# Kernel tuning notes

Measured on AMD Instinct MI355X. Metric: run time of the kernel, lower is better.

Reference implementation:

```python
import jax, jax.numpy as jnp
import numpy as np

BATCH = 512
HIDDEN_DIM = 4096
NUM_CODES = 32
CODE_DIM = 64
CODEBOOK_SIZE = 1024


def _lsa_single(cost):
    """Rectangular Hungarian (Jonker-Volgenant shortest augmenting path).
    cost: [n, m] with n <= m. Returns, for each row, the assigned column,
    minimizing total cost (matches scipy.optimize.linear_sum_assignment)."""
    n, m = cost.shape
    u = np.zeros(n + 1)
    v = np.zeros(m + 1)
    p = np.zeros(m + 1, dtype=np.int64)  # p[j]: row matched to col j (1-based); 0 = free
    for i in range(1, n + 1):
        p[0] = i
        j0 = 0
        minv = np.full(m + 1, np.inf)
        way = np.zeros(m + 1, dtype=np.int64)
        used = np.zeros(m + 1, dtype=bool)
        while True:
            used[j0] = True
            i0 = p[j0]
            free = ~used
            free[0] = False
            jfree = np.nonzero(free)[0]
            cur = cost[i0 - 1, jfree - 1] - u[i0] - v[jfree]
            upd = cur < minv[jfree]
            minv[jfree[upd]] = cur[upd]
            way[jfree[upd]] = j0
            k = jfree[np.argmin(minv[jfree])]
            delta = minv[k]
            u[p[used]] += delta
            v[used] -= delta
            minv[free] -= delta
            j0 = k
            if p[j0] == 0:
                break
        while j0 != 0:  # augment along the path
            j1 = way[j0]
            p[j0] = p[j1]
            j0 = j1
    ans = np.empty(n, dtype=np.int64)
    for j in range(1, m + 1):
        if p[j] > 0:
            ans[p[j] - 1] = j - 1
    return ans


def _lsa_batch(costs):
    costs = np.asarray(costs, dtype=np.float64)
    return np.stack([_lsa_single(c) for c in costs]).astype(np.int32)


def setup_inputs() -> dict:
    key = jax.random.key(0)
    ks = jax.random.split(key, 4)
    return {
        "x": jax.random.normal(ks[0], (BATCH, HIDDEN_DIM), jnp.float32),
        "codebook": jax.random.normal(ks[1], (CODEBOOK_SIZE, CODE_DIM), jnp.float32),
        "enc_w": jax.random.normal(ks[2], (NUM_CODES * CODE_DIM, HIDDEN_DIM), jnp.float32) * 0.02,
        "enc_b": jnp.zeros((NUM_CODES * CODE_DIM,), jnp.float32),
        "dec_w": jax.random.normal(ks[3], (HIDDEN_DIM, NUM_CODES * CODE_DIM), jnp.float32) * 0.02,
        "dec_b": jnp.zeros((HIDDEN_DIM,), jnp.float32),
    }


def reference(x, codebook, enc_w, enc_b, dec_w, dec_b):
    bs = x.shape[0]
    # encoder (torch Linear: y = x @ W.T + b)
    e = (x @ enc_w.T + enc_b).reshape(bs, NUM_CODES, CODE_DIM)
    ef = e.reshape(-1, CODE_DIM)  # [bs*num_codes, code_dim]
    # pairwise Euclidean distances to codebook entries [bs*num_codes, codebook_size]
    d2 = (jnp.sum(ef * ef, axis=1, keepdims=True)
          + jnp.sum(codebook * codebook, axis=1)
          - 2.0 * (ef @ codebook.T))
    dist = jnp.sqrt(jnp.maximum(d2, 0.0)).reshape(bs, NUM_CODES, CODEBOOK_SIZE)
    # per-sample Hungarian assignment (original uses scipy on CPU; sqrt is
    # monotone so the optimal assignment is identical)
    indices = jax.pure_callback(
        _lsa_batch,
        jax.ShapeDtypeStruct((bs, NUM_CODES), jnp.int32),
        jax.lax.stop_gradient(dist),
    )
    flat_idx = indices.reshape(-1)  # matches torch's concatenated flat indices
    q = codebook[flat_idx].reshape(bs, NUM_CODES, CODE_DIM)
    # straight-through estimator
    q_st = e + jax.lax.stop_gradient(q - e)
    r = q_st.reshape(bs, NUM_CODES * CODE_DIM) @ dec_w.T + dec_b
    return (r, q, e, flat_idx)
```

## Files before the change

### kernel.cpp

```cpp
#include <hip/hip_runtime.h>
#include <hip/hip_bf16.h>
#include <stdint.h>

#define BATCH 512
#define HID   4096
#define NC    32
#define CD    64
#define CB    1024
#define NCD   2048

typedef unsigned short u16;
typedef unsigned int   u32;
typedef __attribute__((ext_vector_type(8))) short short8;
typedef __attribute__((ext_vector_type(4))) float f32x4;

#define WAVE_SYNC()  asm volatile("s_waitcnt lgkmcnt(0)" ::: "memory")
#define SCHED_FENCE() __builtin_amdgcn_sched_barrier(0)

__device__ inline u16 bf16_rne(float f) {
  u32 u = __builtin_bit_cast(u32, f);
  u32 r = u + 0x7FFFu + ((u >> 16) & 1u);
  return (u16)(r >> 16);
}
__device__ inline float bf16_f32(u16 h) {
  u32 u = ((u32)h) << 16;
  return __builtin_bit_cast(float, u);
}
__device__ inline void split3(float a, u16& h1, u16& h2, u16& h3) {
  h1 = bf16_rne(a);
  float r1 = a - bf16_f32(h1);
  h2 = bf16_rne(r1);
  float r2 = r1 - bf16_f32(h2);
  h3 = bf16_rne(r2);
}
__device__ inline f32x4 mfma16(short8 a, short8 b, f32x4 c) {
  return __builtin_amdgcn_mfma_f32_16x16x32_bf16(a, b, c, 0, 0, 0);
}
__device__ inline void gload_lds16(const u16* g, u16* l) {
  __builtin_amdgcn_global_load_lds(
      (const __attribute__((address_space(1))) u32*)(const void*)g,
      (__attribute__((address_space(3))) u32*)(void*)l, 16, 0, 0);
}

union H8 { u16 h[8]; short8 v; };

template<int K>
__global__ __launch_bounds__(256) void conv_split3(
    const float* __restrict__ src, u16* __restrict__ d1,
    u16* __restrict__ d2, u16* __restrict__ d3) {
  __shared__ float st[4][16][36];
  const int t = threadIdx.x;
  const int wv = t >> 6, l = t & 63;
  const int g = blockIdx.x * 4 + wv;
  const int rowbase = (g / (K / 32)) * 16;
  const int kbase   = (g % (K / 32)) * 32;
  {
    const float* s = src + (size_t)(rowbase + (l >> 2)) * K + kbase + (l & 3) * 8;
    *(f32x4*)&st[wv][l >> 2][(l & 3) * 8]     = *(const f32x4*)s;
    *(f32x4*)&st[wv][l >> 2][(l & 3) * 8 + 4] = *(const f32x4*)(s + 4);
  }
  __syncthreads();
  float vv[8];
  *(f32x4*)&vv[0] = *(const f32x4*)&st[wv][l & 15][(l >> 4) * 8];
  *(f32x4*)&vv[4] = *(const f32x4*)&st[wv][l & 15][(l >> 4) * 8 + 4];
  H8 o1, o2, o3;
#pragma unroll
  for (int i = 0; i < 8; ++i) split3(vv[i], o1.h[i], o2.h[i], o3.h[i]);
  size_t off = (size_t)g * 512 + l * 8;
  *(short8*)(d1 + off) = o1.v;
  *(short8*)(d2 + off) = o2.v;
  *(short8*)(d3 + off) = o3.v;
}

template<int K>
__global__ __launch_bounds__(256) void conv_split1(
    const float* __restrict__ src, u16* __restrict__ d1) {
  __shared__ float st[4][16][36];
  const int t = threadIdx.x;
  const int wv = t >> 6, l = t & 63;
  const int g = blockIdx.x * 4 + wv;
  const int rowbase = (g / (K / 32)) * 16;
  const int kbase   = (g % (K / 32)) * 32;
  {
    const float* s = src + (size_t)(rowbase + (l >> 2)) * K + kbase + (l & 3) * 8;
    *(f32x4*)&st[wv][l >> 2][(l & 3) * 8]     = *(const f32x4*)s;
    *(f32x4*)&st[wv][l >> 2][(l & 3) * 8 + 4] = *(const f32x4*)(s + 4);
  }
  __syncthreads();
  float vv[8];
  *(f32x4*)&vv[0] = *(const f32x4*)&st[wv][l & 15][(l >> 4) * 8];
  *(f32x4*)&vv[4] = *(const f32x4*)&st[wv][l & 15][(l >> 4) * 8 + 4];
  H8 o1;
#pragma unroll
  for (int i = 0; i < 8; ++i) o1.h[i] = bf16_rne(vv[i]);
  *(short8*)(d1 + (size_t)g * 512 + l * 8) = o1.v;
}

__global__ __launch_bounds__(256, 2) void k1_gemm(
    const u16* __restrict__ A1, const u16* __restrict__ A2,
    const u16* __restrict__ A3,
    const u16* __restrict__ B1, const u16* __restrict__ B2,
    const u16* __restrict__ B3, float* __restrict__ part) {
  __shared__ u16 lds_all[72 * 512];
  const int t = threadIdx.x;
  const int wid = t >> 6, lane = t & 63;
  const int wrow = wid >> 1, wcol = wid & 1;
  const int d = blockIdx.x + (blockIdx.y << 2) + (blockIdx.z << 7);
  const int xcd = d & 7, sl = d >> 3;
  const int panel = (xcd << 4) + (sl >> 2);
  const int bm = (sl & 3) * 128;
  const int bn_t = panel & 31;
  const int kz = panel >> 5;
  const int ks0 = kz * 32;

  const u16* gp[9];
#pragma unroll
  for (int i = 0; i < 9; ++i) {
    const int b = wid + 4 * i;
    const u16* base;
    size_t frag;
    if (b < 24) {
      const int s = b >> 3, rf = b & 7;
      base = (s == 0) ? A1 : (s == 1) ? A2 : A3;
      frag = (size_t)((bm >> 4) + rf);
    } else {
      const int bb = b - 24;
      const int s = bb >> 2, cf = bb & 3;
      base = (s == 0) ? B1 : (s == 1) ? B2 : B3;
      frag = (size_t)(bn_t * 4 + cf);
    }
    gp[i] = base + (frag * 128 + ks0) * 512 + lane * 8;
  }

  f32x4 acc[4][2];
#pragma unroll
  for (int r = 0; r < 4; ++r)
#pragma unroll
    for (int c = 0; c < 2; ++c) acc[r][c] = (f32x4)0.f;

  for (int ks = 0; ks < 16; ++ks) {
#pragma unroll
    for (int i = 0; i < 9; ++i) {
      const int b = wid + 4 * i;
      gload_lds16(gp[i],       &lds_all[b * 512]);
      gload_lds16(gp[i] + 512, &lds_all[(36 + b) * 512]);
      gp[i] += 1024;
    }
    __syncthreads();
#pragma unroll
    for (int ss = 0; ss < 2; ++ss) {
      const int o = ss * 36;
      short8 b0[2], b1[2], b2[2];
#pragma unroll
      for (int c = 0; c < 2; ++c) {
        const int cf = wcol * 2 + c;
        b0[c] = *(const short8*)&lds_all[(o + 24 + 0 * 4 + cf) * 512 + lane * 8];
        b1[c] = *(const short8*)&lds_all[(o + 24 + 1 * 4 + cf) * 512 + lane * 8];
        b2[c] = *(const short8*)&lds_all[(o + 24 + 2 * 4 + cf) * 512 + lane * 8];
      }
#pragma unroll
      for (int r = 0; r < 4; ++r) {
        const int rf = wrow * 4 + r;
        short8 a0 = *(const short8*)&lds_all[(o + 0 * 8 + rf) * 512 + lane * 8];
        short8 a1 = *(const short8*)&lds_all[(o + 1 * 8 + rf) * 512 + lane * 8];
        short8 a2 = *(const short8*)&lds_all[(o + 2 * 8 + rf) * 512 + lane * 8];
#pragma unroll
        for (int c = 0; c < 2; ++c) {
          f32x4 dd = acc[r][c];
          dd = mfma16(a0, b0[c], dd);
          dd = mfma16(a0, b1[c], dd);
          dd = mfma16(a1, b0[c], dd);
          dd = mfma16(a1, b1[c], dd);
          dd = mfma16(a0, b2[c], dd);
          dd = mfma16(a2, b0[c], dd);
          acc[r][c] = dd;
        }
      }
    }
    __syncthreads();
  }
  float* P = part + (size_t)kz * BATCH * NCD;
#pragma unroll
  for (int r = 0; r < 4; ++r)
#pragma unroll
    for (int c = 0; c < 2; ++c) {
      int row = bm + wrow * 64 + r * 16 + (lane >> 4) * 4;
      int col = bn_t * 64 + wcol * 32 + c * 16 + (lane & 15);
#pragma unroll
      for (int i = 0; i < 4; ++i)
        P[(size_t)(row + i) * NCD + col] = acc[r][c][i];
    }
}

__global__ __launch_bounds__(256) void k_reduce_bias(
    const float* __restrict__ part, const float* __restrict__ bias,
    float* __restrict__ e) {
  size_t o = ((size_t)blockIdx.x * 256 + threadIdx.x) * 4;
  int n = (int)(o & (NCD - 1));
  f32x4 s = *(const f32x4*)(part + o);
  s += *(const f32x4*)(part + (size_t)1 * BATCH * NCD + o);
  s += *(const f32x4*)(part + (size_t)2 * BATCH * NCD + o);
  s += *(const f32x4*)(part + (size_t)3 * BATCH * NCD + o);
  s += *(const f32x4*)(bias + n);
  *(f32x4*)(e + o) = s;
}

__global__ __launch_bounds__(512) void k3_gemm(
    const u16* __restrict__ Ab, const u16* __restrict__ Bb,
    const float* __restrict__ bias, float* __restrict__ C) {
  __shared__ u16 As[4][64][8];
  __shared__ u16 Bs[8][64][8];
  const int t = threadIdx.x;
  const int wid = t >> 6, lane = t & 63;
  const int wrow = wid >> 2, wcol = wid & 3;
  const int d = blockIdx.x + (blockIdx.y << 3);
  const int xcd = d & 7, sl = d >> 3;
  const int bn = ((xcd << 2) + (sl >> 3)) * 128;
  const int bm = (sl & 7) * 64;
  f32x4 acc[2][2];
#pragma unroll
  for (int r = 0; r < 2; ++r)
#pragma unroll
    for (int c = 0; c < 2; ++c) acc[r][c] = (f32x4)0.f;

  for (int ks = 0; ks < 64; ++ks) {
    {
      size_t gb = (((size_t)(bn >> 4) + wid) * 64 + ks) * 512 + lane * 8;
      gload_lds16(Bb + gb, &Bs[wid][0][0]);
      if (wid < 4) {
        size_t ga = (((size_t)(bm >> 4) + wid) * 64 + ks) * 512 + lane * 8;
        gload_lds16(Ab + ga, &As[wid][0][0]);
      }
    }
    __syncthreads();
    short8 a[2], b[2];
#pragma unroll
    for (int r = 0; r < 2; ++r) a[r] = *(const short8*)&As[wrow * 2 + r][lane][0];
#pragma unroll
    for (int c = 0; c < 2; ++c) b[c] = *(const short8*)&Bs[wcol * 2 + c][lane][0];
#pragma unroll
    for (int r = 0; r < 2; ++r)
#pragma unroll
      for (int c = 0; c < 2; ++c) acc[r][c] = mfma16(a[r], b[c], acc[r][c]);
    __syncthreads();
  }
#pragma unroll
  for (int r = 0; r < 2; ++r)
#pragma unroll
    for (int c = 0; c < 2; ++c) {
      int row = bm + wrow * 32 + r * 16 + (lane >> 4) * 4;
      int col = bn + wcol * 32 + c * 16 + (lane & 15);
      float bb = bias[col];
#pragma unroll
      for (int i = 0; i < 4; ++i)
        C[(size_t)(row + i) * HID + col] = acc[r][c][i] + bb;
    }
}

__global__ __launch_bounds__(512) void k_cost(
    const float* __restrict__ e_glob,
    const float* __restrict__ codebook,
    float* __restrict__ cost) {
  __shared__ u16 Ea[2][3][8][64][8];
  __shared__ u16 Cbs[2][3][8][64][8];
  __shared__ float enorm[128], cnorm[128];
  const int t = threadIdx.x;
  const int wid = t >> 6, lane = t & 63;
  const int wrow = wid >> 2, wcol = wid & 3;
  const int r0 = blockIdx.x * 128;
  const int c0 = blockIdx.y * 128;

  {
    const int fr = lane & 15, kc = lane >> 4;
    const float* ea = e_glob   + (size_t)(r0 + wid * 16 + fr) * CD + kc * 8;
    const float* cb = codebook + (size_t)(c0 + wid * 16 + fr) * CD + kc * 8;
#pragma unroll
    for (int ks = 0; ks < 2; ++ks) {
      float va[8], vb[8];
      *(f32x4*)&va[0] = *(const f32x4*)(ea + ks * 32);
      *(f32x4*)&va[4] = *(const f32x4*)(ea + ks * 32 + 4);
      *(f32x4*)&vb[0] = *(const f32x4*)(cb + ks * 32);
      *(f32x4*)&vb[4] = *(const f32x4*)(cb + ks * 32 + 4);
      H8 a1, a2, a3, b1, b2, b3;
#pragma unroll
      for (int i = 0; i < 8; ++i) {
        split3(va[i], a1.h[i], a2.h[i], a3.h[i]);
        split3(vb[i], b1.h[i], b2.h[i], b3.h[i]);
      }
      *(short8*)&Ea[ks][0][wid][lane][0] = a1.v;
      *(short8*)&Ea[ks][1][wid][lane][0] = a2.v;
      *(short8*)&Ea[ks][2][wid][lane][0] = a3.v;
      *(short8*)&Cbs[ks][0][wid][lane][0] = b1.v;
      *(short8*)&Cbs[ks][1][wid][lane][0] = b2.v;
      *(short8*)&Cbs[ks][2][wid][lane][0] = b3.v;
    }
  }
  if (t < 256) {
    const int which = t >> 7, idx = t & 127;
    const float* p = which ? codebook + (size_t)(c0 + idx) * CD
                           : e_glob   + (size_t)(r0 + idx) * CD;
    float s = 0.f;
#pragma unroll
    for (int k = 0; k < 16; ++k) {
      f32x4 v = *(const f32x4*)(p + k * 4);
      s += v.x * v.x + v.y * v.y + v.z * v.z + v.w * v.w;
    }
    if (which) cnorm[idx] = s; else enorm[idx] = s;
  }
  __syncthreads();

  f32x4 acc[4][2];
#pragma unroll
  for (int r = 0; r < 4; ++r)
#pragma unroll
    for (int c = 0; c < 2; ++c) acc[r][c] = (f32x4)0.f;
#pragma unroll
  for (int ks = 0; ks < 2; ++ks) {
    short8 a0[4], a1[4], a2[4], b0[2], b1[2], b2[2];
#pragma unroll
    for (int r = 0; r < 4; ++r) {
      a0[r] = *(const short8*)&Ea[ks][0][wrow * 4 + r][lane][0];
      a1[r] = *(const short8*)&Ea[ks][1][wrow * 4 + r][lane][0];
      a2[r] = *(const short8*)&Ea[ks][2][wrow * 4 + r][lane][0];
    }
#pragma unroll
    for (int c = 0; c < 2; ++c) {
      b0[c] = *(const short8*)&Cbs[ks][0][wcol * 2 + c][lane][0];
      b1[c] = *(const short8*)&Cbs[ks][1][wcol * 2 + c][lane][0];
      b2[c] = *(const short8*)&Cbs[ks][2][wcol * 2 + c][lane][0];
    }
#pragma unroll
    for (int r = 0; r < 4; ++r)
#pragma unroll
      for (int c = 0; c < 2; ++c) {
        f32x4 dd = acc[r][c];
        dd = mfma16(a0[r], b0[c], dd);
        dd = mfma16(a0[r], b1[c], dd);
        dd = mfma16(a1[r], b0[c], dd);
        dd = mfma16(a1[r], b1[c], dd);
        dd = mfma16(a0[r], b2[c], dd);
        dd = mfma16(a2[r], b0[c], dd);
        acc[r][c] = dd;
      }
  }
#pragma unroll
  for (int r = 0; r < 4; ++r)
#pragma unroll
    for (int c = 0; c < 2; ++c) {
      const int rl = wrow * 64 + r * 16 + (lane >> 4) * 4;
      const int cl = wcol * 32 + c * 16 + (lane & 15);
      const float cn = cnorm[cl];
#pragma unroll
      for (int i = 0; i < 4; ++i) {
        float d2 = enorm[rl + i] + cn - 2.f * acc[r][c][i];
        cost[(size_t)(r0 + rl + i) * CB + c0 + cl] = sqrtf(fmaxf(d2, 0.f));
      }
    }
}

__global__ __launch_bounds__(64, 1) void k_assign(
    const float* __restrict__ cost_g, const float* __restrict__ codebook,
    float* __restrict__ q_out, float* __restrict__ idx_out) {
  __shared__ int idxl[32];
  const int lane = threadIdx.x;
  const int s = blockIdx.x;
  const float* __restrict__ cost = cost_g + (size_t)s * NC * CB;

  double v_[16], minv_[16];
  u32 wp_[16];
  double u_val = 0.0;
#pragma unroll
  for (int r = 0; r < 16; ++r) { v_[r] = 0.0; wp_[r] = 0; }

  float pf[16];
#pragma unroll
  for (int r = 0; r < 16; ++r) pf[r] = cost[r * 64 + lane];

  for (int i = 1; i <= NC; ++i) {
#pragma unroll
    for (int r = 0; r < 16; ++r) minv_[r] = 1e300;
    u32 col_used = 0;
    unsigned long long rowmask = 0ull;
    int j0 = 0;
    int i0 = i;
    float cc[16];
#pragma unroll
    for (int r = 0; r < 16; ++r) cc[r] = pf[r];
    int first = 1;
    for (int guard = 0; guard < 1056; ++guard) {
      rowmask |= (1ull << i0);
      const double ui0 = __shfl(u_val, i0);
      if (first && i < NC) {
#pragma unroll
        for (int r = 0; r < 16; ++r)
          pf[r] = cost[(size_t)i * CB + r * 64 + lane];
      }
      first = 0;
      double bv = 1e301; int bj = 1 << 20;
#pragma unroll
      for (int r = 0; r < 16; ++r) {
        const int j = 1 + lane + r * 64;
        if (!((col_used >> r) & 1u)) {
          double cur = (double)cc[r] - ui0 - v_[r];
          if (cur < minv_[r]) { minv_[r] = cur; wp_[r] = (wp_[r] & 0xFFFF0000u) | (u32)j0; }
          if (minv_[r] < bv) { bv = minv_[r]; bj = j; }
        }
      }
#pragma unroll
      for (int off = 1; off < 64; off <<= 1) {
        double ov = __shfl_xor(bv, off);
        int oj = __shfl_xor(bj, off);
        if (ov < bv || (ov == bv && oj < bj)) { bv = ov; bj = oj; }
      }
      const double delta = bv;
      const int k = bj;
      const int rk = (k - 1) >> 6, kl = (k - 1) & 63;
      u32 sel = 0;
#pragma unroll
      for (int r = 0; r < 16; ++r) if (r == rk) sel = wp_[r];
      const int pmk = ((u32)__shfl((int)sel, kl)) >> 16;
      float ccn[16];
      if (pmk > 0) {
        const float* crow = cost + (size_t)(pmk - 1) * CB;
#pragma unroll
        for (int r = 0; r < 16; ++r) ccn[r] = crow[r * 64 + lane];
      }
      if ((rowmask >> lane) & 1ull) u_val += delta;
#pragma unroll
      for (int r = 0; r < 16; ++r) {
        const int j = 1 + lane + r * 64;
        if ((col_used >> r) & 1u) v_[r] -= delta;
        else {
          minv_[r] -= delta;
          if (j == k) col_used |= (1u << r);
        }
      }
      j0 = k;
      if (pmk == 0) break;
      i0 = pmk;
#pragma unroll
      for (int r = 0; r < 16; ++r) cc[r] = ccn[r];
    }
    int jj = j0;
    while (jj != 0) {
      const int rj = (jj - 1) >> 6, lj = (jj - 1) & 63;
      u32 wsel = 0;
#pragma unroll
      for (int r = 0; r < 16; ++r) if (r == rj) wsel = wp_[r];
      const int j1 = ((u32)__shfl((int)wsel, lj)) & 0xFFFFu;
      int newpm;
      if (j1 == 0) newpm = i;
      else {
        const int r1 = (j1 - 1) >> 6, l1 = (j1 - 1) & 63;
        u32 psel = 0;
#pragma unroll
        for (int r = 0; r < 16; ++r) if (r == r1) psel = wp_[r];
        newpm = ((u32)__shfl((int)psel, l1)) >> 16;
      }
#pragma unroll
      for (int r = 0; r < 16; ++r)
        if (lane == lj && r == rj) wp_[r] = (wp_[r] & 0xFFFFu) | ((u32)newpm << 16);
      jj = j1;
    }
  }

#pragma unroll
  for (int r = 0; r < 16; ++r) {
    const u32 pm = wp_[r] >> 16;
    if (pm > 0) idxl[pm - 1] = lane + r * 64;
  }
  WAVE_SYNC(); SCHED_FENCE();
  if (lane < NC) idx_out[(size_t)s * NC + lane] = (float)idxl[lane];
#pragma unroll
  for (int p = 0; p < 8; ++p) {
    int vi = p * 64 + lane;
    int r = vi >> 4, c4 = vi & 15;
    int ci = idxl[r];
    float4 qv = *(const float4*)&codebook[(size_t)ci * 64 + c4 * 4];
    *(float4*)&q_out[(size_t)s * NCD + r * 64 + c4 * 4] = qv;
  }
}

extern "C" void kernel_launch(void* const* d_in, const int* in_sizes, int n_in,
                              void* d_out, int out_size, void* d_ws, size_t ws_size,
                              hipStream_t stream) {
  (void)in_sizes; (void)n_in; (void)out_size; (void)ws_size;
  const float* x        = (const float*)d_in[0];
  const float* codebook = (const float*)d_in[1];
  const float* enc_w    = (const float*)d_in[2];
  const float* enc_b    = (const float*)d_in[3];
  const float* dec_w    = (const float*)d_in[4];
  const float* dec_b    = (const float*)d_in[5];

  float* out = (float*)d_out;
  float* r_out   = out;
  float* q_out   = out + 2097152;
  float* e_out   = out + 2097152 + 1048576;
  float* idx_out = out + 2097152 + 2097152;

  char* ws = (char*)d_ws;
  u16* B1 = (u16*)ws;
  u16* B2 = (u16*)(ws + (16u << 20));
  u16* B3 = (u16*)(ws + (32u << 20));
  float* part = (float*)(ws + (48u << 20));
  float* cost_ws = (float*)ws;
  u16* qb  = (u16*)ws;
  u16* dwb = (u16*)(ws + (2u << 20));
  u16* A1 = (u16*)r_out;
  u16* A2 = (u16*)r_out + 2097152;
  u16* A3 = (u16*)q_out;

  conv_split3<HID><<<1024, 256, 0, stream>>>(x, A1, A2, A3);
  conv_split3<HID><<<4096, 256, 0, stream>>>(enc_w, B1, B2, B3);
  k1_gemm<<<dim3(4, 32, 4), 256, 0, stream>>>(A1, A2, A3, B1, B2, B3, part);
  k_reduce_bias<<<1024, 256, 0, stream>>>(part, enc_b, e_out);
  k_cost<<<dim3(128, 8), 512, 0, stream>>>(e_out, codebook, cost_ws);
  k_assign<<<BATCH, 64, 0, stream>>>(cost_ws, codebook, q_out, idx_out);
  conv_split1<NCD><<<4096, 256, 0, stream>>>(dec_w, dwb);
  conv_split1<NCD><<<512, 256, 0, stream>>>(q_out, qb);
  k3_gemm<<<dim3(8, 32), 512, 0, stream>>>(qb, dwb, dec_b, r_out);
}
```

Baseline: 214.4 us.

## Double-buffer k1_gemm LDS loads and merge bf16 conversion launches

Restructures the encoder GEMM main loop so the next K-slice is prefetched into a second LDS buffer while MFMAs run on the current one. It uses a single sync per 32-wide step instead of loading two sub-slices and computing them after one barrier. The two conv_split1 launches for dec_w and q are merged into one dual-source kernel to save a launch. Per-step work is halved and the loop count doubled, so barrier count stays the same while load latency may be hidden better.

```diff
diff --git a/kernel.cpp b/kernel.cpp
--- a/kernel.cpp
+++ b/kernel.cpp
@@ -72,17 +72,20 @@
   *(short8*)(d3 + off) = o3.v;
 }
 
-template<int K>
-__global__ __launch_bounds__(256) void conv_split1(
-    const float* __restrict__ src, u16* __restrict__ d1) {
+__global__ __launch_bounds__(256) void conv_split1_dual(
+    const float* __restrict__ s1, u16* __restrict__ dst1,
+    const float* __restrict__ s2, u16* __restrict__ dst2) {
   __shared__ float st[4][16][36];
   const int t = threadIdx.x;
   const int wv = t >> 6, l = t & 63;
-  const int g = blockIdx.x * 4 + wv;
-  const int rowbase = (g / (K / 32)) * 16;
-  const int kbase   = (g % (K / 32)) * 32;
+  const int bb = blockIdx.x;
+  const float* src; u16* dst; int g;
+  if (bb < 4096) { src = s1; dst = dst1; g = bb * 4 + wv; }
+  else           { src = s2; dst = dst2; g = (bb - 4096) * 4 + wv; }
+  const int rowbase = (g / 64) * 16;
+  const int kbase   = (g % 64) * 32;
   {
-    const float* s = src + (size_t)(rowbase + (l >> 2)) * K + kbase + (l & 3) * 8;
+    const float* s = src + (size_t)(rowbase + (l >> 2)) * 2048 + kbase + (l & 3) * 8;
     *(f32x4*)&st[wv][l >> 2][(l & 3) * 8]     = *(const f32x4*)s;
     *(f32x4*)&st[wv][l >> 2][(l & 3) * 8 + 4] = *(const f32x4*)(s + 4);
   }
@@ -93,7 +96,7 @@
   H8 o1;
 #pragma unroll
   for (int i = 0; i < 8; ++i) o1.h[i] = bf16_rne(vv[i]);
-  *(short8*)(d1 + (size_t)g * 512 + l * 8) = o1.v;
+  *(short8*)(dst + (size_t)g * 512 + l * 8) = o1.v;
 }
 
 __global__ __launch_bounds__(256, 2) void k1_gemm(
@@ -101,7 +104,7 @@
     const u16* __restrict__ A3,
     const u16* __restrict__ B1, const u16* __restrict__ B2,
     const u16* __restrict__ B3, float* __restrict__ part) {
-  __shared__ u16 lds_all[72 * 512];
+  __shared__ u16 lds_all[2][36 * 512];
   const int t = threadIdx.x;
   const int wid = t >> 6, lane = t & 63;
   const int wrow = wid >> 1, wcol = wid & 1;
@@ -138,43 +141,46 @@
 #pragma unroll
     for (int c = 0; c < 2; ++c) acc[r][c] = (f32x4)0.f;
 
-  for (int ks = 0; ks < 16; ++ks) {
-#pragma unroll
-    for (int i = 0; i < 9; ++i) {
-      const int b = wid + 4 * i;
-      gload_lds16(gp[i],       &lds_all[b * 512]);
-      gload_lds16(gp[i] + 512, &lds_all[(36 + b) * 512]);
-      gp[i] += 1024;
-    }
-    __syncthreads();
-#pragma unroll
-    for (int ss = 0; ss < 2; ++ss) {
-      const int o = ss * 36;
-      short8 b0[2], b1[2], b2[2];
+#pragma unroll
+  for (int i = 0; i < 9; ++i) {
+    gload_lds16(gp[i], &lds_all[0][(wid + 4 * i) * 512]);
+    gp[i] += 512;
+  }
+  __syncthreads();
+
+  for (int ks = 0; ks < 32; ++ks) {
+    const int cur = ks & 1, nxt = cur ^ 1;
+    if (ks < 31) {
+#pragma unroll
+      for (int i = 0; i < 9; ++i) {
+        gload_lds16(gp[i], &lds_all[nxt][(wid + 4 * i) * 512]);
+        gp[i] += 512;
+      }
+    }
+    short8 b0[2], b1[2], b2[2];
+#pragma unroll
+    for (int c = 0; c < 2; ++c) {
+      const int cf = wcol * 2 + c;
+      b0[c] = *(const short8*)&lds_all[cur][(24 + 0 * 4 + cf) * 512 + lane * 8];
+      b1[c] = *(const short8*)&lds_all[cur][(24 + 1 * 4 + cf) * 512 + lane * 8];
+      b2[c] = *(const short8*)&lds_all[cur][(24 + 2 * 4 + cf) * 512 + lane * 8];
+    }
+#pragma unroll
+    for (int r = 0; r < 4; ++r) {
+      const int rf = wrow * 4 + r;
+      short8 a0 = *(const short8*)&lds_all[cur][(0 * 8 + rf) * 512 + lane * 8];
+      short8 a1 = *(const short8*)&lds_all[cur][(1 * 8 + rf) * 512 + lane * 8];
+      short8 a2 = *(const short8*)&lds_all[cur][(2 * 8 + rf) * 512 + lane * 8];
 #pragma unroll
       for (int c = 0; c < 2; ++c) {
-        const int cf = wcol * 2 + c;
-        b0[c] = *(const short8*)&lds_all[(o + 24 + 0 * 4 + cf) * 512 + lane * 8];
-        b1[c] = *(const short8*)&lds_all[(o + 24 + 1 * 4 + cf) * 512 + lane * 8];
-        b2[c] = *(const short8*)&lds_all[(o + 24 + 2 * 4 + cf) * 512 + lane * 8];
-      }
-#pragma unroll
-      for (int r = 0; r < 4; ++r) {
-        const int rf = wrow * 4 + r;
-        short8 a0 = *(const short8*)&lds_all[(o + 0 * 8 + rf) * 512 + lane * 8];
-        short8 a1 = *(const short8*)&lds_all[(o + 1 * 8 + rf) * 512 + lane * 8];
-        short8 a2 = *(const short8*)&lds_all[(o + 2 * 8 + rf) * 512 + lane * 8];
-#pragma unroll
-        for (int c = 0; c < 2; ++c) {
-          f32x4 dd = acc[r][c];
-          dd = mfma16(a0, b0[c], dd);
-          dd = mfma16(a0, b1[c], dd);
-          dd = mfma16(a1, b0[c], dd);
-          dd = mfma16(a1, b1[c], dd);
-          dd = mfma16(a0, b2[c], dd);
-          dd = mfma16(a2, b0[c], dd);
-          acc[r][c] = dd;
-        }
+        f32x4 dd = acc[r][c];
+        dd = mfma16(a0, b0[c], dd);
+        dd = mfma16(a0, b1[c], dd);
+        dd = mfma16(a1, b0[c], dd);
+        dd = mfma16(a1, b1[c], dd);
+        dd = mfma16(a0, b2[c], dd);
+        dd = mfma16(a2, b0[c], dd);
+        acc[r][c] = dd;
       }
     }
     __syncthreads();
@@ -516,7 +522,6 @@
   k_reduce_bias<<<1024, 256, 0, stream>>>(part, enc_b, e_out);
   k_cost<<<dim3(128, 8), 512, 0, stream>>>(e_out, codebook, cost_ws);
   k_assign<<<BATCH, 64, 0, stream>>>(cost_ws, codebook, q_out, idx_out);
-  conv_split1<NCD><<<4096, 256, 0, stream>>>(dec_w, dwb);
-  conv_split1<NCD><<<512, 256, 0, stream>>>(q_out, qb);
+  conv_split1_dual<<<4608, 256, 0, stream>>>(dec_w, dwb, q_out, qb);
   k3_gemm<<<dim3(8, 32), 512, 0, stream>>>(qb, dwb, dec_b, r_out);
 }
```

Measured after the change: 211.7 us. Within noise of the previous version (-1.3%).
